# Kernel tuning notes

Measured on AMD Instinct MI355X. Metric: run time of the kernel, lower is better.

## Reference

```python
import jax, jax.numpy as jnp
import numpy as np

N_MEMORY = 16
FEA_DIM = 512


def setup_inputs() -> dict:
    key = jax.random.key(0)
    ks = jax.random.split(key, 8)
    b, L, d, n = 4, 4096, FEA_DIM, N_MEMORY
    scale = 1.0 / np.sqrt(d)  # ~ torch Linear default init scale
    return {
        "query": jax.random.normal(ks[0], (b, L, d), dtype=jnp.float32),
        "W1": jax.random.uniform(ks[1], (n, d, d), jnp.float32, -scale, scale),
        "b1": jax.random.uniform(ks[2], (n, d), jnp.float32, -scale, scale),
        "W2": jax.random.uniform(ks[3], (n, d, d), jnp.float32, -scale, scale),
        "b2": jax.random.uniform(ks[4], (n, d), jnp.float32, -scale, scale),
        "Wg": jax.random.uniform(ks[5], (n, d), jnp.float32, -scale, scale),
        "bg": jax.random.uniform(ks[6], (n,), jnp.float32, -scale, scale),
        "topk": 8,
    }


def reference(query, W1, b1, W2, b2, Wg, bg, topk):
    # query: [b, L, d]; stacked per-memory-slot params: W1/W2 [n, d, d], Wg [n, d]
    n = W1.shape[0]
    # per-slot LeakyReLU negative slopes: 0.01 + 0.2/n * l
    slopes = (0.01 + 0.2 / n * jnp.arange(n, dtype=query.dtype))[:, None, None, None]
    # memory_function: Linear -> LeakyReLU(slope_l) -> Linear -> Tanh, all slots at once
    h = jnp.einsum('bld,ndh->nblh', query, W1) + b1[:, None, None, :]   # [n,b,L,d]
    h = jnp.where(h >= 0, h, h * slopes)
    x = jnp.tanh(jnp.einsum('nblh,nhd->nbld', h, W2) + b2[:, None, None, :])  # [n,b,L,d]
    # gate: Linear(d,1) -> softmax over L -> topk over L -> gather -> weighted sum
    logits = jnp.einsum('nbld,nd->nbl', x, Wg) + bg[:, None, None]      # [n,b,L]
    w = jax.nn.softmax(logits, axis=-1)
    top_w, top_idx = jax.lax.top_k(w, topk)                             # [n,b,k]
    items = jnp.take_along_axis(x, top_idx[..., None], axis=2)          # [n,b,k,d]
    combined = jnp.einsum('nbkd,nbk->nbd', items, top_w)                # [n,b,d]
    m_item = jnp.transpose(combined, (1, 0, 2))                         # [b,n,d]
    # F.normalize(dim=-1), eps=1e-12
    norm = jnp.maximum(jnp.linalg.norm(m_item, axis=-1, keepdims=True), 1e-12)
    return m_item / norm
```

## Files before the change

### kernel.cpp

```cpp
#include <hip/hip_runtime.h>
#include <hip/hip_bf16.h>
#include <cstdint>
#include <cstddef>

#define NMEM 16
#define DDIM 512
#define BATCH 4
#define LSEQ 4096
#define ROWS 16384
#define NCAND 32
#define KTOP 8
#define QPAD 20

typedef __attribute__((ext_vector_type(4))) float f32x4;
typedef __attribute__((ext_vector_type(16))) float f32x16;
typedef __attribute__((ext_vector_type(8))) int int8v;

__device__ inline void gld16(const void* gptr, void* lptr) {
    __builtin_amdgcn_global_load_lds(
        (const __attribute__((address_space(1))) unsigned int*)gptr,
        (__attribute__((address_space(3))) unsigned int*)lptr,
        16, 0, 0);
}

__device__ inline float fast_tanh(float x) {
    float t = __builtin_amdgcn_fmed3f(x, -3.f, 3.f);
    float t2 = t * t;
    return t * (27.f + t2) * __builtin_amdgcn_rcpf(27.f + 9.f * t2);
}

__device__ inline int8v ldg_frag(const unsigned char* p) {
    int4 x = *(const int4*)p;
    int4 y = *(const int4*)(p + 16);
    int8v v;
    v[0] = x.x; v[1] = x.y; v[2] = x.z; v[3] = x.w;
    v[4] = y.x; v[5] = y.y; v[6] = y.z; v[7] = y.w;
    return v;
}

__device__ inline int8v load_frag_half(const unsigned char* Ts, int row, int kh) {
    int key = (row >> 1) & 3;
    const int4* p0 = (const int4*)(Ts + row * 64 + ((((kh << 1) | 0) ^ key) << 4));
    const int4* p1 = (const int4*)(Ts + row * 64 + ((((kh << 1) | 1) ^ key) << 4));
    int4 x = *p0, y = *p1;
    int8v v;
    v[0] = x.x; v[1] = x.y; v[2] = x.z; v[3] = x.w;
    v[4] = y.x; v[5] = y.y; v[6] = y.z; v[7] = y.w;
    return v;
}

__device__ inline void stage_half(const unsigned char* Wbase, unsigned char* dst,
                                  int tid) {
    #pragma unroll
    for (int i = 0; i < 2; ++i) {
        int c = i * 256 + tid;
        int row = c >> 2, s = c & 3;
        gld16(Wbase + (size_t)row * DDIM + ((s ^ ((row >> 1) & 3)) << 4),
              dst + c * 16);
    }
}

__global__ __launch_bounds__(256)
void prep_kernel(const float* __restrict__ query,
                 const float* __restrict__ W1, const float* __restrict__ W2,
                 unsigned char* __restrict__ Q8,
                 unsigned char* __restrict__ W1T8, unsigned char* __restrict__ W2T8) {
    int blk = blockIdx.x, t = threadIdx.x;
    if (blk < 2048) {
        size_t base = ((size_t)blk * 256 + t) * 16;
        const float4* in = (const float4*)(query + base);
        int4 o; int* op = (int*)&o;
        #pragma unroll
        for (int q = 0; q < 4; ++q) {
            float4 v = in[q];
            int lo = __builtin_amdgcn_cvt_pk_fp8_f32(v.x, v.y, 0, false);
            op[q] = __builtin_amdgcn_cvt_pk_fp8_f32(v.z, v.w, lo, true);
        }
        *(int4*)(Q8 + base) = o;
    } else {
        __shared__ float tile[64][69];
        int bid = blk - 2048;
        const float* Win = W1; unsigned char* Wout = W1T8;
        if (bid >= 1024) { bid -= 1024; Win = W2; Wout = W2T8; }
        int n = bid >> 6, t64 = bid & 63;
        int dt = (t64 >> 3) << 6, jt = (t64 & 7) << 6;
        const float* inN = Win + (size_t)n * DDIM * DDIM;
        unsigned char* outN = Wout + (size_t)n * DDIM * DDIM;
        int rr = t >> 4, cc = (t & 15) * 4;
        #pragma unroll
        for (int pass = 0; pass < 4; ++pass) {
            int row = rr + pass * 16;
            float4 v = *(const float4*)(inN + (size_t)(dt + row) * DDIM + jt + cc);
            tile[row][cc] = v.x; tile[row][cc + 1] = v.y;
            tile[row][cc + 2] = v.z; tile[row][cc + 3] = v.w;
        }
        __syncthreads();
        #pragma unroll
        for (int pass = 0; pass < 4; ++pass) {
            int jl = rr + pass * 16;
            float f0 = tile[cc][jl], f1 = tile[cc + 1][jl];
            float f2 = tile[cc + 2][jl], f3 = tile[cc + 3][jl];
            int lo = __builtin_amdgcn_cvt_pk_fp8_f32(f0, f1, 0, false);
            int dw = __builtin_amdgcn_cvt_pk_fp8_f32(f2, f3, lo, true);
            *(int*)(outN + (size_t)(jt + jl) * DDIM + dt + cc) = dw;
        }
    }
}

__global__ __launch_bounds__(256, 2)
void fused_mlp_kernel(const unsigned char* __restrict__ Q8,
                      const unsigned char* __restrict__ W1T8,
                      const unsigned char* __restrict__ W2T8,
                      const float* __restrict__ b1, const float* __restrict__ b2,
                      const float* __restrict__ Wg,
                      float* __restrict__ logits)
{
    __shared__ unsigned char hbuf[128 * 512];
    __shared__ unsigned char Bs[2][8192];
    const int id = blockIdx.x;
    const int n = id & 15;
    const int m0 = (id >> 4) * 128;
    const int tid = threadIdx.x, lane = tid & 63;
    const int w = tid >> 6;
    const int rh = w >> 1, ch = w & 1;
    const int l31 = lane & 31, kh = lane >> 5;
    const unsigned char* W1n = W1T8 + (size_t)n * DDIM * DDIM;
    const unsigned char* W2n = W2T8 + (size_t)n * DDIM * DDIM;
    const float slope = 0.01f + 0.0125f * n;
    const unsigned char* Aq0 = Q8 + (size_t)(m0 + rh * 64 + l31) * DDIM + kh * 32;

    int8v avc0 = ldg_frag(Aq0);
    int8v avc1 = ldg_frag(Aq0 + (size_t)32 * DDIM);
    stage_half(W1n, Bs[0], tid);
    __syncthreads();

    #pragma unroll 1
    for (int n0 = 0; n0 < 4; ++n0) {
        f32x16 acc[2][2] = {};
        #pragma unroll 1
        for (int p8 = 0; p8 < 8; ++p8) {
            int q  = n0 * 8 + p8;
            int qn = q + 1;
            const unsigned char* nsrc =
                (qn == 32) ? W2n
                           : W1n + (size_t)((qn >> 3) * 128) * DDIM + (qn & 7) * 64;
            stage_half(nsrc, Bs[qn & 1], tid);
            int qa = qn & 7;
            int8v avn0 = ldg_frag(Aq0 + qa * 64);
            int8v avn1 = ldg_frag(Aq0 + (size_t)32 * DDIM + qa * 64);
            const unsigned char* Ts = Bs[q & 1];
            #pragma unroll
            for (int fc = 0; fc < 2; ++fc) {
                int8v wfr = load_frag_half(Ts, ch * 64 + fc * 32 + l31, kh);
                acc[0][fc] = __builtin_amdgcn_mfma_scale_f32_32x32x64_f8f6f4(
                    wfr, avc0, acc[0][fc], 0, 0, 0, 0x7F7F7F7F, 0, 0x7F7F7F7F);
                acc[1][fc] = __builtin_amdgcn_mfma_scale_f32_32x32x64_f8f6f4(
                    wfr, avc1, acc[1][fc], 0, 0, 0, 0x7F7F7F7F, 0, 0x7F7F7F7F);
            }
            avc0 = avn0; avc1 = avn1;
            __syncthreads();
        }
        #pragma unroll
        for (int fc = 0; fc < 2; ++fc) {
            #pragma unroll
            for (int rt = 0; rt < 2; ++rt) {
                int r = rh * 64 + rt * 32 + l31;
                #pragma unroll
                for (int q = 0; q < 4; ++q) {
                    int jb = n0 * 128 + ch * 64 + fc * 32 + 8 * q + 4 * kh;
                    float4 bias = *(const float4*)(b1 + n * DDIM + jb);
                    float v0 = acc[rt][fc][4 * q + 0] + bias.x;
                    float v1 = acc[rt][fc][4 * q + 1] + bias.y;
                    float v2 = acc[rt][fc][4 * q + 2] + bias.z;
                    float v3 = acc[rt][fc][4 * q + 3] + bias.w;
                    v0 = v0 >= 0.f ? v0 : v0 * slope;
                    v1 = v1 >= 0.f ? v1 : v1 * slope;
                    v2 = v2 >= 0.f ? v2 : v2 * slope;
                    v3 = v3 >= 0.f ? v3 : v3 * slope;
                    int lo = __builtin_amdgcn_cvt_pk_fp8_f32(v0, v1, 0, false);
                    int dw = __builtin_amdgcn_cvt_pk_fp8_f32(v2, v3, lo, true);
                    *(int*)(hbuf + r * 512 + ((((jb >> 4) ^ (r & 7)) << 4) | (jb & 15))) = dw;
                }
            }
        }
    }

    __syncthreads();

    float rowacc[2][16] = {};
    #pragma unroll 1
    for (int n0 = 0; n0 < 4; ++n0) {
        f32x16 acc[2][2] = {};
        #pragma unroll 1
        for (int p8 = 0; p8 < 8; ++p8) {
            int q  = n0 * 8 + p8;
            int qn = q + 1;
            if (qn < 32)
                stage_half(W2n + (size_t)((qn >> 3) * 128) * DDIM + (qn & 7) * 64,
                           Bs[qn & 1], tid);
            int C0 = p8 * 4 + 2 * kh;
            int8v hv0, hv1;
            {
                int hrow = rh * 64 + l31, hq = hrow & 7;
                const int4* p0 = (const int4*)(hbuf + hrow * 512 + ((C0 ^ hq) << 4));
                const int4* p1 = (const int4*)(hbuf + hrow * 512 + (((C0 + 1) ^ hq) << 4));
                int4 x = *p0, y = *p1;
                hv0[0] = x.x; hv0[1] = x.y; hv0[2] = x.z; hv0[3] = x.w;
                hv0[4] = y.x; hv0[5] = y.y; hv0[6] = y.z; hv0[7] = y.w;
            }
            {
                int hrow = rh * 64 + 32 + l31, hq = hrow & 7;
                const int4* p0 = (const int4*)(hbuf + hrow * 512 + ((C0 ^ hq) << 4));
                const int4* p1 = (const int4*)(hbuf + hrow * 512 + (((C0 + 1) ^ hq) << 4));
                int4 x = *p0, y = *p1;
                hv1[0] = x.x; hv1[1] = x.y; hv1[2] = x.z; hv1[3] = x.w;
                hv1[4] = y.x; hv1[5] = y.y; hv1[6] = y.z; hv1[7] = y.w;
            }
            const unsigned char* Ts = Bs[q & 1];
            #pragma unroll
            for (int fc = 0; fc < 2; ++fc) {
                int8v wfr = load_frag_half(Ts, ch * 64 + fc * 32 + l31, kh);
                acc[0][fc] = __builtin_amdgcn_mfma_scale_f32_32x32x64_f8f6f4(
                    hv0, wfr, acc[0][fc], 0, 0, 0, 0x7F7F7F7F, 0, 0x7F7F7F7F);
                acc[1][fc] = __builtin_amdgcn_mfma_scale_f32_32x32x64_f8f6f4(
                    hv1, wfr, acc[1][fc], 0, 0, 0, 0x7F7F7F7F, 0, 0x7F7F7F7F);
            }
            __syncthreads();
        }
        #pragma unroll
        for (int fc = 0; fc < 2; ++fc) {
            int j = n0 * 128 + ch * 64 + fc * 32 + l31;
            float bias = b2[n * DDIM + j];
            float wgv = Wg[n * DDIM + j];
            #pragma unroll
            for (int rt = 0; rt < 2; ++rt)
                #pragma unroll
                for (int reg = 0; reg < 16; ++reg)
                    rowacc[rt][reg] = fmaf(fast_tanh(acc[rt][fc][reg] + bias), wgv,
                                           rowacc[rt][reg]);
        }
    }
    #pragma unroll
    for (int sh = 1; sh < 32; sh <<= 1)
        #pragma unroll
        for (int rt = 0; rt < 2; ++rt)
            #pragma unroll
            for (int reg = 0; reg < 16; ++reg)
                rowacc[rt][reg] += __shfl_xor(rowacc[rt][reg], sh);
    __syncthreads();
    float* lsum = (float*)hbuf;
    if (l31 == 0) {
        #pragma unroll
        for (int rt = 0; rt < 2; ++rt)
            #pragma unroll
            for (int reg = 0; reg < 16; ++reg)
                lsum[ch * 128 + rh * 64 + rt * 32 + (reg & 3) + 8 * (reg >> 2) + 4 * kh]
                    = rowacc[rt][reg];
    }
    __syncthreads();
    if (tid < 128)
        logits[(size_t)n * ROWS + m0 + tid] = lsum[tid] + lsum[128 + tid];
}

__global__ __launch_bounds__(256)
void topcand_kernel(const float* __restrict__ logits, int* __restrict__ cand,
                    float* __restrict__ ex_logit) {
    __shared__ float lv[LSEQ];
    __shared__ float cv[128];
    __shared__ int   ci[128];
    int p = blockIdx.x, n = p >> 2, b = p & 3;
    int t = threadIdx.x, lane = t & 63, w = t >> 6;
    const float* L = logits + (size_t)n * ROWS + (size_t)b * LSEQ;
    for (int i = t; i < LSEQ; i += 256) lv[i] = L[i];
    __syncthreads();
    float mv[16];
    int base = w * 1024;
    #pragma unroll
    for (int j = 0; j < 16; ++j) mv[j] = lv[base + j * 64 + lane];
    for (int rd = 0; rd < 32; ++rd) {
        float best = mv[0]; int bj = 0;
        #pragma unroll
        for (int j = 1; j < 16; ++j)
            if (mv[j] > best) { best = mv[j]; bj = j; }
        int bidx = base + bj * 64 + lane;
        float rv = best; int ridx = bidx;
        #pragma unroll
        for (int s = 1; s < 64; s <<= 1) {
            float ov = __shfl_xor(rv, s); int oi = __shfl_xor(ridx, s);
            if (ov > rv || (ov == rv && oi < ridx)) { rv = ov; ridx = oi; }
        }
        if (lane == 0) { cv[w * 32 + rd] = rv; ci[w * 32 + rd] = ridx; }
        if (ridx == bidx) mv[bj] = -1e30f;
    }
    __syncthreads();
    if (w == 0) {
        float v2[2]; int i2[2];
        #pragma unroll
        for (int k = 0; k < 2; ++k) { v2[k] = cv[k * 64 + lane]; i2[k] = ci[k * 64 + lane]; }
        for (int rd = 0; rd < 32; ++rd) {
            float best = v2[0]; int bi = i2[0]; int bk = 0;
            if (v2[1] > best || (v2[1] == best && i2[1] < bi)) { best = v2[1]; bi = i2[1]; bk = 1; }
            float rv = best; int ridx = bi;
            #pragma unroll
            for (int s = 1; s < 64; s <<= 1) {
                float ov = __shfl_xor(rv, s); int oi = __shfl_xor(ridx, s);
                if (ov > rv || (ov == rv && oi < ridx)) { rv = ov; ridx = oi; }
            }
            if (lane == 0) cand[p * NCAND + rd] = ridx;
            if (ridx == bi) v2[bk] = -1e30f;
        }
    } else if (w == 1) {
        if (lane < NCAND) ex_logit[p * NCAND + lane] = 0.f;
    }
}

__global__ __launch_bounds__(256)
void exact_h_kernel(const float* __restrict__ query,
                    const float* __restrict__ W1, const float* __restrict__ b1,
                    const int* __restrict__ cand, float* __restrict__ ex_h) {
    __shared__ float qs[DDIM][QPAD];
    __shared__ float hpart[4][16][64];
    int blk = blockIdx.x;
    int p = blk >> 4, r4 = blk & 15;
    int ct = r4 >> 3, jc = r4 & 7;
    int n = p >> 2, b = p & 3;
    int t = threadIdx.x, jj = t & 63, dg = t >> 6;
    int j = jc * 64 + jj;
    for (int c = 0; c < 16; ++c) {
        int li = cand[p * NCAND + ct * 16 + c];
        const float* qr = query + ((size_t)b * LSEQ + li) * DDIM;
        for (int d = t; d < DDIM; d += 256) qs[d][c] = qr[d];
    }
    __syncthreads();
    const float* W1n = W1 + (size_t)n * DDIM * DDIM;
    float acc[16] = {};
    for (int d = dg * 128; d < dg * 128 + 128; ++d) {
        float wvv = W1n[(size_t)d * DDIM + j];
        const float4* qv = (const float4*)&qs[d][0];
        #pragma unroll
        for (int c4 = 0; c4 < 4; ++c4) {
            float4 q4 = qv[c4];
            acc[c4 * 4 + 0] = fmaf(q4.x, wvv, acc[c4 * 4 + 0]);
            acc[c4 * 4 + 1] = fmaf(q4.y, wvv, acc[c4 * 4 + 1]);
            acc[c4 * 4 + 2] = fmaf(q4.z, wvv, acc[c4 * 4 + 2]);
            acc[c4 * 4 + 3] = fmaf(q4.w, wvv, acc[c4 * 4 + 3]);
        }
    }
    #pragma unroll
    for (int c = 0; c < 16; ++c) hpart[dg][c][jj] = acc[c];
    __syncthreads();
    const float slope = 0.01f + 0.0125f * n;
    float bias = b1[n * DDIM + j];
    for (int cc = dg; cc < 16; cc += 4) {
        float h = hpart[0][cc][jj] + hpart[1][cc][jj] + hpart[2][cc][jj]
                + hpart[3][cc][jj] + bias;
        h = h >= 0.f ? h : h * slope;
        ex_h[((size_t)p * NCAND + ct * 16 + cc) * DDIM + j] = h;
    }
}

__global__ __launch_bounds__(256)
void exact_x_kernel(const float* __restrict__ ex_h,
                    const float* __restrict__ W2, const float* __restrict__ b2,
                    const float* __restrict__ Wg,
                    float* __restrict__ ex_x, float* __restrict__ ex_logit) {
    __shared__ float hs[DDIM][QPAD];
    __shared__ float xpart[4][16][64];
    int blk = blockIdx.x;
    int p = blk >> 4, r4 = blk & 15;
    int ct = r4 >> 3, jc = r4 & 7;
    int n = p >> 2;
    int t = threadIdx.x, jj = t & 63, dg = t >> 6;
    int j = jc * 64 + jj;
    for (int c = 0; c < 16; ++c) {
        const float* hr = ex_h + ((size_t)p * NCAND + ct * 16 + c) * DDIM;
        for (int d = t; d < DDIM; d += 256) hs[d][c] = hr[d];
    }
    __syncthreads();
    const float* W2n = W2 + (size_t)n * DDIM * DDIM;
    float acc[16] = {};
    for (int d = dg * 128; d < dg * 128 + 128; ++d) {
        float wvv = W2n[(size_t)d * DDIM + j];
        const float4* hv = (const float4*)&hs[d][0];
        #pragma unroll
        for (int c4 = 0; c4 < 4; ++c4) {
            float4 h4 = hv[c4];
            acc[c4 * 4 + 0] = fmaf(h4.x, wvv, acc[c4 * 4 + 0]);
            acc[c4 * 4 + 1] = fmaf(h4.y, wvv, acc[c4 * 4 + 1]);
            acc[c4 * 4 + 2] = fmaf(h4.z, wvv, acc[c4 * 4 + 2]);
            acc[c4 * 4 + 3] = fmaf(h4.w, wvv, acc[c4 * 4 + 3]);
        }
    }
    #pragma unroll
    for (int c = 0; c < 16; ++c) xpart[dg][c][jj] = acc[c];
    __syncthreads();
    float bias = b2[n * DDIM + j];
    float wg = Wg[n * DDIM + j];
    for (int cc = dg; cc < 16; cc += 4) {
        float a = xpart[0][cc][jj] + xpart[1][cc][jj] + xpart[2][cc][jj]
                + xpart[3][cc][jj] + bias;
        float x = tanhf(a);
        ex_x[((size_t)p * NCAND + ct * 16 + cc) * DDIM + j] = x;
        float lp = x * wg;
        #pragma unroll
        for (int s = 1; s < 64; s <<= 1) lp += __shfl_xor(lp, s);
        if (jj == 0) atomicAdd(&ex_logit[p * NCAND + ct * 16 + cc], lp);
    }
}

__global__ __launch_bounds__(64)
void final_kernel(const float* __restrict__ ex_x, const float* __restrict__ ex_logit,
                  const int* __restrict__ cand, float* __restrict__ out)
{
    __shared__ float w8s[KTOP];
    __shared__ int   s8s[KTOP];
    int p = blockIdx.x, n = p >> 2, b = p & 3;
    int t = threadIdx.x;
    float myv = (t < NCAND) ? ex_logit[p * NCAND + t] : -1e30f;
    int myidx = (t < NCAND) ? cand[p * NCAND + t] : 0x7fffffff;
    float lmax = 0.f;
    for (int k = 0; k < KTOP; ++k) {
        float rv = myv; int ridx = myidx; int rl = t;
        #pragma unroll
        for (int s = 1; s < 64; s <<= 1) {
            float ov = __shfl_xor(rv, s); int oi = __shfl_xor(ridx, s); int ol = __shfl_xor(rl, s);
            if (ov > rv || (ov == rv && oi < ridx)) { rv = ov; ridx = oi; rl = ol; }
        }
        if (k == 0) lmax = rv;
        if (t == 0) { w8s[k] = __expf(rv - lmax); s8s[k] = rl; }
        if (t == rl) myv = -1e30f;
    }
    __syncthreads();
    float cvv[8];
    float sq = 0.f;
    int idx = 0;
    for (int d = t; d < DDIM; d += 64, ++idx) {
        float s = 0.f;
        #pragma unroll
        for (int k = 0; k < KTOP; ++k)
            s = fmaf(w8s[k], ex_x[((size_t)p * NCAND + s8s[k]) * DDIM + d], s);
        cvv[idx] = s;
        sq += s * s;
    }
    #pragma unroll
    for (int s = 1; s < 64; s <<= 1) sq += __shfl_xor(sq, s);
    float norm = fmaxf(sqrtf(sq), 1e-12f);
    idx = 0;
    for (int d = t; d < DDIM; d += 64, ++idx)
        out[((size_t)b * NMEM + n) * DDIM + d] = cvv[idx] / norm;
}

extern "C" void kernel_launch(void* const* d_in, const int* in_sizes, int n_in,
                              void* d_out, int out_size, void* d_ws, size_t ws_size,
                              hipStream_t stream)
{
    const float* query = (const float*)d_in[0];
    const float* W1    = (const float*)d_in[1];
    const float* b1    = (const float*)d_in[2];
    const float* W2    = (const float*)d_in[3];
    const float* b2    = (const float*)d_in[4];
    const float* Wg    = (const float*)d_in[5];

    char* ws = (char*)d_ws;
    const size_t MB = 1024 * 1024;
    unsigned char* Q8   = (unsigned char*)(ws);
    unsigned char* W1T8 = (unsigned char*)(ws + 8 * MB);
    unsigned char* W2T8 = (unsigned char*)(ws + 12 * MB);
    float* logits   = (float*)(ws + 16 * MB);
    int*   cand     = (int*)  (ws + 17 * MB);
    float* ex_logit = (float*)(ws + 17 * MB + 16384);
    float* ex_h     = (float*)(ws + 20 * MB);
    float* ex_x     = (float*)(ws + 28 * MB);

    prep_kernel<<<4096, 256, 0, stream>>>(query, W1, W2, Q8, W1T8, W2T8);
    fused_mlp_kernel<<<2048, 256, 0, stream>>>(Q8, W1T8, W2T8, b1, b2, Wg, logits);
    topcand_kernel<<<64, 256, 0, stream>>>(logits, cand, ex_logit);
    exact_h_kernel<<<1024, 256, 0, stream>>>(query, W1, b1, cand, ex_h);
    exact_x_kernel<<<1024, 256, 0, stream>>>(ex_h, W2, b2, Wg, ex_x, ex_logit);
    final_kernel<<<64, 64, 0, stream>>>(ex_x, ex_logit, cand, (float*)d_out);
}
```

Before: 505.1 us.

## Halve fused MLP row tile and deepen weight staging to four buffers

The fused MLP kernel's row tile drops from 128 to 64 rows per block, doubling the grid. The whole Q fragment row is now preloaded into registers up front. Weight staging moves from two to four LDS buffers with a prefetch distance of three, and the full __syncthreads is replaced by partial vmcnt waits plus s_barrier. The aim is to shrink LDS use so more blocks fit per CU and to hide global-load latency better. The cost is that each weight tile is staged from global memory twice as often, so weight traffic per row doubles and MFMA reuse per staged tile drops.

```diff
diff --git a/kernel.cpp b/kernel.cpp
--- a/kernel.cpp
+++ b/kernel.cpp
@@ -115,11 +115,12 @@
                       const float* __restrict__ Wg,
                       float* __restrict__ logits)
 {
-    __shared__ unsigned char hbuf[128 * 512];
-    __shared__ unsigned char Bs[2][8192];
+    __shared__ unsigned char hbuf[64 * 512];
+    __shared__ unsigned char Bs[4][8192];
+    __shared__ float lsum[2][64];
     const int id = blockIdx.x;
     const int n = id & 15;
-    const int m0 = (id >> 4) * 128;
+    const int m0 = (id >> 4) * 64;
     const int tid = threadIdx.x, lane = tid & 63;
     const int w = tid >> 6;
     const int rh = w >> 1, ch = w & 1;
@@ -127,105 +128,96 @@
     const unsigned char* W1n = W1T8 + (size_t)n * DDIM * DDIM;
     const unsigned char* W2n = W2T8 + (size_t)n * DDIM * DDIM;
     const float slope = 0.01f + 0.0125f * n;
-    const unsigned char* Aq0 = Q8 + (size_t)(m0 + rh * 64 + l31) * DDIM + kh * 32;
-
-    int8v avc0 = ldg_frag(Aq0);
-    int8v avc1 = ldg_frag(Aq0 + (size_t)32 * DDIM);
-    stage_half(W1n, Bs[0], tid);
-    __syncthreads();
+    const unsigned char* Aq0 = Q8 + (size_t)(m0 + rh * 32 + l31) * DDIM + kh * 32;
+
+    int8v avq[8];
+    #pragma unroll
+    for (int qa = 0; qa < 8; ++qa)
+        avq[qa] = ldg_frag(Aq0 + qa * 64);
+    stage_half(W1n,       Bs[0], tid);
+    stage_half(W1n + 64,  Bs[1], tid);
+    stage_half(W1n + 128, Bs[2], tid);
+    asm volatile("s_waitcnt vmcnt(4)" ::: "memory");
+    __builtin_amdgcn_s_barrier();
+    __builtin_amdgcn_sched_barrier(0);
 
     #pragma unroll 1
     for (int n0 = 0; n0 < 4; ++n0) {
-        f32x16 acc[2][2] = {};
+        f32x16 acc[2] = {};
+        #pragma unroll
+        for (int p8 = 0; p8 < 8; ++p8) {
+            const int P = n0 * 8 + p8, Pn = P + 3;
+            const unsigned char* nsrc = (Pn < 32)
+                ? W1n + (size_t)((Pn >> 3) * 128) * DDIM + (Pn & 7) * 64
+                : W2n + (size_t)(((Pn - 32) >> 3) * 128) * DDIM + ((Pn - 32) & 7) * 64;
+            stage_half(nsrc, Bs[Pn & 3], tid);
+            const unsigned char* Ts = Bs[P & 3];
+            int8v wfr0 = load_frag_half(Ts, ch * 64 + l31, kh);
+            int8v wfr1 = load_frag_half(Ts, ch * 64 + 32 + l31, kh);
+            acc[0] = __builtin_amdgcn_mfma_scale_f32_32x32x64_f8f6f4(
+                wfr0, avq[p8], acc[0], 0, 0, 0, 0x7F7F7F7F, 0, 0x7F7F7F7F);
+            acc[1] = __builtin_amdgcn_mfma_scale_f32_32x32x64_f8f6f4(
+                wfr1, avq[p8], acc[1], 0, 0, 0, 0x7F7F7F7F, 0, 0x7F7F7F7F);
+            asm volatile("s_waitcnt vmcnt(4)" ::: "memory");
+            __builtin_amdgcn_s_barrier();
+            __builtin_amdgcn_sched_barrier(0);
+        }
+        #pragma unroll
+        for (int fc = 0; fc < 2; ++fc) {
+            int r = rh * 32 + l31;
+            #pragma unroll
+            for (int q = 0; q < 4; ++q) {
+                int jb = n0 * 128 + ch * 64 + fc * 32 + 8 * q + 4 * kh;
+                float4 bias = *(const float4*)(b1 + n * DDIM + jb);
+                float v0 = acc[fc][4 * q + 0] + bias.x;
+                float v1 = acc[fc][4 * q + 1] + bias.y;
+                float v2 = acc[fc][4 * q + 2] + bias.z;
+                float v3 = acc[fc][4 * q + 3] + bias.w;
+                v0 = v0 >= 0.f ? v0 : v0 * slope;
+                v1 = v1 >= 0.f ? v1 : v1 * slope;
+                v2 = v2 >= 0.f ? v2 : v2 * slope;
+                v3 = v3 >= 0.f ? v3 : v3 * slope;
+                int lo = __builtin_amdgcn_cvt_pk_fp8_f32(v0, v1, 0, false);
+                int dw = __builtin_amdgcn_cvt_pk_fp8_f32(v2, v3, lo, true);
+                *(int*)(hbuf + r * 512 + ((((jb >> 4) ^ (r & 7)) << 4) | (jb & 15))) = dw;
+            }
+        }
+    }
+
+    __syncthreads();
+
+    float rowacc[16] = {};
+    #pragma unroll 1
+    for (int n0 = 0; n0 < 4; ++n0) {
+        f32x16 acc[2] = {};
         #pragma unroll 1
         for (int p8 = 0; p8 < 8; ++p8) {
-            int q  = n0 * 8 + p8;
-            int qn = q + 1;
-            const unsigned char* nsrc =
-                (qn == 32) ? W2n
-                           : W1n + (size_t)((qn >> 3) * 128) * DDIM + (qn & 7) * 64;
-            stage_half(nsrc, Bs[qn & 1], tid);
-            int qa = qn & 7;
-            int8v avn0 = ldg_frag(Aq0 + qa * 64);
-            int8v avn1 = ldg_frag(Aq0 + (size_t)32 * DDIM + qa * 64);
-            const unsigned char* Ts = Bs[q & 1];
-            #pragma unroll
-            for (int fc = 0; fc < 2; ++fc) {
-                int8v wfr = load_frag_half(Ts, ch * 64 + fc * 32 + l31, kh);
-                acc[0][fc] = __builtin_amdgcn_mfma_scale_f32_32x32x64_f8f6f4(
-                    wfr, avc0, acc[0][fc], 0, 0, 0, 0x7F7F7F7F, 0, 0x7F7F7F7F);
-                acc[1][fc] = __builtin_amdgcn_mfma_scale_f32_32x32x64_f8f6f4(
-                    wfr, avc1, acc[1][fc], 0, 0, 0, 0x7F7F7F7F, 0, 0x7F7F7F7F);
-            }
-            avc0 = avn0; avc1 = avn1;
-            __syncthreads();
-        }
-        #pragma unroll
-        for (int fc = 0; fc < 2; ++fc) {
-            #pragma unroll
-            for (int rt = 0; rt < 2; ++rt) {
-                int r = rh * 64 + rt * 32 + l31;
-                #pragma unroll
-                for (int q = 0; q < 4; ++q) {
-                    int jb = n0 * 128 + ch * 64 + fc * 32 + 8 * q + 4 * kh;
-                    float4 bias = *(const float4*)(b1 + n * DDIM + jb);
-                    float v0 = acc[rt][fc][4 * q + 0] + bias.x;
-                    float v1 = acc[rt][fc][4 * q + 1] + bias.y;
-                    float v2 = acc[rt][fc][4 * q + 2] + bias.z;
-                    float v3 = acc[rt][fc][4 * q + 3] + bias.w;
-                    v0 = v0 >= 0.f ? v0 : v0 * slope;
-                    v1 = v1 >= 0.f ? v1 : v1 * slope;
-                    v2 = v2 >= 0.f ? v2 : v2 * slope;
-                    v3 = v3 >= 0.f ? v3 : v3 * slope;
-                    int lo = __builtin_amdgcn_cvt_pk_fp8_f32(v0, v1, 0, false);
-                    int dw = __builtin_amdgcn_cvt_pk_fp8_f32(v2, v3, lo, true);
-                    *(int*)(hbuf + r * 512 + ((((jb >> 4) ^ (r & 7)) << 4) | (jb & 15))) = dw;
-                }
-            }
-        }
-    }
-
-    __syncthreads();
-
-    float rowacc[2][16] = {};
-    #pragma unroll 1
-    for (int n0 = 0; n0 < 4; ++n0) {
-        f32x16 acc[2][2] = {};
-        #pragma unroll 1
-        for (int p8 = 0; p8 < 8; ++p8) {
-            int q  = n0 * 8 + p8;
-            int qn = q + 1;
-            if (qn < 32)
-                stage_half(W2n + (size_t)((qn >> 3) * 128) * DDIM + (qn & 7) * 64,
-                           Bs[qn & 1], tid);
+            const int P = 32 + n0 * 8 + p8, Pn = P + 3;
+            if (Pn < 64)
+                stage_half(W2n + (size_t)(((Pn - 32) >> 3) * 128) * DDIM
+                               + ((Pn - 32) & 7) * 64,
+                           Bs[Pn & 3], tid);
+            int hrow = rh * 32 + l31, hq = hrow & 7;
             int C0 = p8 * 4 + 2 * kh;
-            int8v hv0, hv1;
+            int8v hv;
             {
-                int hrow = rh * 64 + l31, hq = hrow & 7;
                 const int4* p0 = (const int4*)(hbuf + hrow * 512 + ((C0 ^ hq) << 4));
                 const int4* p1 = (const int4*)(hbuf + hrow * 512 + (((C0 + 1) ^ hq) << 4));
                 int4 x = *p0, y = *p1;
-                hv0[0] = x.x; hv0[1] = x.y; hv0[2] = x.z; hv0[3] = x.w;
-                hv0[4] = y.x; hv0[5] = y.y; hv0[6] = y.z; hv0[7] = y.w;
+                hv[0] = x.x; hv[1] = x.y; hv[2] = x.z; hv[3] = x.w;
+                hv[4] = y.x; hv[5] = y.y; hv[6] = y.z; hv[7] = y.w;
             }
-            {
-                int hrow = rh * 64 + 32 + l31, hq = hrow & 7;
-                const int4* p0 = (const int4*)(hbuf + hrow * 512 + ((C0 ^ hq) << 4));
-                const int4* p1 = (const int4*)(hbuf + hrow * 512 + (((C0 + 1) ^ hq) << 4));
-                int4 x = *p0, y = *p1;
-                hv1[0] = x.x; hv1[1] = x.y; hv1[2] = x.z; hv1[3] = x.w;
-                hv1[4] = y.x; hv1[5] = y.y; hv1[6] = y.z; hv1[7] = y.w;
-            }
-            const unsigned char* Ts = Bs[q & 1];
-            #pragma unroll
-            for (int fc = 0; fc < 2; ++fc) {
-                int8v wfr = load_frag_half(Ts, ch * 64 + fc * 32 + l31, kh);
-                acc[0][fc] = __builtin_amdgcn_mfma_scale_f32_32x32x64_f8f6f4(
-                    hv0, wfr, acc[0][fc], 0, 0, 0, 0x7F7F7F7F, 0, 0x7F7F7F7F);
-                acc[1][fc] = __builtin_amdgcn_mfma_scale_f32_32x32x64_f8f6f4(
-                    hv1, wfr, acc[1][fc], 0, 0, 0, 0x7F7F7F7F, 0, 0x7F7F7F7F);
-            }
-            __syncthreads();
+            const unsigned char* Ts = Bs[P & 3];
+            int8v wfr0 = load_frag_half(Ts, ch * 64 + l31, kh);
+            int8v wfr1 = load_frag_half(Ts, ch * 64 + 32 + l31, kh);
+            acc[0] = __builtin_amdgcn_mfma_scale_f32_32x32x64_f8f6f4(
+                hv, wfr0, acc[0], 0, 0, 0, 0x7F7F7F7F, 0, 0x7F7F7F7F);
+            acc[1] = __builtin_amdgcn_mfma_scale_f32_32x32x64_f8f6f4(
+                hv, wfr1, acc[1], 0, 0, 0, 0x7F7F7F7F, 0, 0x7F7F7F7F);
+            if (Pn < 64) asm volatile("s_waitcnt vmcnt(4)" ::: "memory");
+            else         asm volatile("s_waitcnt vmcnt(0)" ::: "memory");
+            __builtin_amdgcn_s_barrier();
+            __builtin_amdgcn_sched_barrier(0);
         }
         #pragma unroll
         for (int fc = 0; fc < 2; ++fc) {
@@ -233,33 +225,23 @@
             float bias = b2[n * DDIM + j];
             float wgv = Wg[n * DDIM + j];
             #pragma unroll
-            for (int rt = 0; rt < 2; ++rt)
-                #pragma unroll
-                for (int reg = 0; reg < 16; ++reg)
-                    rowacc[rt][reg] = fmaf(fast_tanh(acc[rt][fc][reg] + bias), wgv,
-                                           rowacc[rt][reg]);
+            for (int reg = 0; reg < 16; ++reg)
+                rowacc[reg] = fmaf(fast_tanh(acc[fc][reg] + bias), wgv, rowacc[reg]);
         }
     }
     #pragma unroll
     for (int sh = 1; sh < 32; sh <<= 1)
         #pragma unroll
-        for (int rt = 0; rt < 2; ++rt)
-            #pragma unroll
-            for (int reg = 0; reg < 16; ++reg)
-                rowacc[rt][reg] += __shfl_xor(rowacc[rt][reg], sh);
-    __syncthreads();
-    float* lsum = (float*)hbuf;
+        for (int reg = 0; reg < 16; ++reg)
+            rowacc[reg] += __shfl_xor(rowacc[reg], sh);
     if (l31 == 0) {
         #pragma unroll
-        for (int rt = 0; rt < 2; ++rt)
-            #pragma unroll
-            for (int reg = 0; reg < 16; ++reg)
-                lsum[ch * 128 + rh * 64 + rt * 32 + (reg & 3) + 8 * (reg >> 2) + 4 * kh]
-                    = rowacc[rt][reg];
-    }
-    __syncthreads();
-    if (tid < 128)
-        logits[(size_t)n * ROWS + m0 + tid] = lsum[tid] + lsum[128 + tid];
+        for (int reg = 0; reg < 16; ++reg)
+            lsum[ch][rh * 32 + (reg & 3) + 8 * (reg >> 2) + 4 * kh] = rowacc[reg];
+    }
+    __syncthreads();
+    if (tid < 64)
+        logits[(size_t)n * ROWS + m0 + tid] = lsum[0][tid] + lsum[1][tid];
 }
 
 __global__ __launch_bounds__(256)
@@ -473,7 +455,7 @@
     float* ex_x     = (float*)(ws + 28 * MB);
 
     prep_kernel<<<4096, 256, 0, stream>>>(query, W1, W2, Q8, W1T8, W2T8);
-    fused_mlp_kernel<<<2048, 256, 0, stream>>>(Q8, W1T8, W2T8, b1, b2, Wg, logits);
+    fused_mlp_kernel<<<4096, 256, 0, stream>>>(Q8, W1T8, W2T8, b1, b2, Wg, logits);
     topcand_kernel<<<64, 256, 0, stream>>>(logits, cand, ex_logit);
     exact_h_kernel<<<1024, 256, 0, stream>>>(query, W1, b1, cand, ex_h);
     exact_x_kernel<<<1024, 256, 0, stream>>>(ex_h, W2, b2, Wg, ex_x, ex_logit);
```

Result: faster. 487.3 us (-3.5%).
